# Kernel optimization log

Measured on AMD Instinct MI355X. Metric: run time of the kernel, lower is better.

The kernel has to match this reference:

```python
import jax, jax.numpy as jnp
import numpy as np

B, E, H, NC = 16384, 1024, 8, 32
FF = 4 * E

def _ln(x, g, b, eps=1e-5):
    m = jnp.mean(x, -1, keepdims=True)
    v = jnp.mean((x - m) ** 2, -1, keepdims=True)
    return (x - m) * jax.lax.rsqrt(v + eps) * g + b

def _mha1(q_in, kv_in, Wq, Wk, Wv, bq, bk, bv, Wo, bo):
    # seq_len == 1 for both query and key/value; x: [B, E]
    Bn = q_in.shape[0]
    dh = E // H
    q = (q_in @ Wq.T + bq).reshape(Bn, H, dh)
    k = (kv_in @ Wk.T + bk).reshape(Bn, H, dh)
    v = (kv_in @ Wv.T + bv).reshape(Bn, H, dh)
    s = jnp.sum(q * k, -1, keepdims=True) / np.float32(np.sqrt(dh))  # [B,H,1]
    w = jax.nn.softmax(s, axis=-1)  # single key -> weights == 1 exactly
    o = (w * v).reshape(Bn, E)
    return o @ Wo.T + bo

def _ffn(x, W1, b1, W2, b2):
    h = jax.nn.gelu(x @ W1.T + b1, approximate=False)  # torch GELU = exact erf
    return h @ W2.T + b2

def setup_inputs():
    key = jax.random.key(0)
    ks = iter(jax.random.split(key, 64))
    def w(shape, s=0.02):
        return jax.random.normal(next(ks), shape, jnp.float32) * s
    z = lambda n: jnp.zeros((n,), jnp.float32)
    o = lambda n: jnp.ones((n,), jnp.float32)
    d = {
        'lc_cls': jax.random.normal(next(ks), (B, E), jnp.float32),
        'tab_embedding': jax.random.normal(next(ks), (B, E), jnp.float32),
        'ln_lc_g': o(E), 'ln_lc_b': z(E),
        'ln_tab_g': o(E), 'ln_tab_b': z(E),
    }
    for p in ('alc', 'atab'):
        d[p + '_Wq'] = w((E, E)); d[p + '_Wk'] = w((E, E)); d[p + '_Wv'] = w((E, E))
        d[p + '_bq'] = z(E); d[p + '_bk'] = z(E); d[p + '_bv'] = z(E)
        d[p + '_Wo'] = w((E, E)); d[p + '_bo'] = z(E)
    for p in ('flc', 'ftab'):
        d[p + '_W1'] = w((FF, E)); d[p + '_b1'] = z(FF)
        d[p + '_W2'] = w((E, FF)); d[p + '_b2'] = z(E)
    d['on_g'] = o(2 * E); d['on_b'] = z(2 * E)
    d['c_W1'] = w((E, 2 * E)); d['c_b1'] = z(E)
    d['c_ln_g'] = o(E); d['c_ln_b'] = z(E)
    d['c_W2'] = w((NC, E)); d['c_b2'] = z(NC)
    return d

def reference(lc_cls, tab_embedding, ln_lc_g, ln_lc_b, ln_tab_g, ln_tab_b,
              alc_Wq, alc_Wk, alc_Wv, alc_bq, alc_bk, alc_bv, alc_Wo, alc_bo,
              atab_Wq, atab_Wk, atab_Wv, atab_bq, atab_bk, atab_bv, atab_Wo, atab_bo,
              flc_W1, flc_b1, flc_W2, flc_b2, ftab_W1, ftab_b1, ftab_W2, ftab_b2,
              on_g, on_b, c_W1, c_b1, c_ln_g, c_ln_b, c_W2, c_b2):
    # dropout is identity at inference
    lc_n = _ln(lc_cls, ln_lc_g, ln_lc_b)
    tab_n = _ln(tab_embedding, ln_tab_g, ln_tab_b)
    lc_cross = lc_cls + _mha1(lc_n, tab_n, alc_Wq, alc_Wk, alc_Wv, alc_bq, alc_bk, alc_bv, alc_Wo, alc_bo)
    tab_cross = tab_embedding + _mha1(tab_n, lc_n, atab_Wq, atab_Wk, atab_Wv, atab_bq, atab_bk, atab_bv, atab_Wo, atab_bo)
    lc_out = lc_cross + _ffn(lc_cross, flc_W1, flc_b1, flc_W2, flc_b2)
    tab_out = tab_cross + _ffn(tab_cross, ftab_W1, ftab_b1, ftab_W2, ftab_b2)
    fused = _ln(jnp.concatenate([lc_out, tab_out], axis=1), on_g, on_b)
    h = jax.nn.gelu(_ln(fused @ c_W1.T + c_b1, c_ln_g, c_ln_b), approximate=False)
    return h @ c_W2.T + c_b2
```

## Files before the change

kernel.cpp:

```cpp
#include <hip/hip_runtime.h>
#include <hip/hip_bf16.h>
#include <math.h>

typedef __bf16 bf16_t;
typedef __bf16 bf16x8 __attribute__((ext_vector_type(8)));
typedef __bf16 bf16x4 __attribute__((ext_vector_type(4)));
typedef float  f32x4  __attribute__((ext_vector_type(4)));

#define NB   16384
#define EDIM 1024
#define FFD  4096
#define NCD  32

__device__ __forceinline__ float gelu_exact(float x) {
    return 0.5f * x * (1.0f + erff(x * 0.70710678118654752f));
}

__device__ __forceinline__ void gload16(const bf16_t* g, bf16_t* l) {
    __builtin_amdgcn_global_load_lds(
        (__attribute__((address_space(1))) void*)(g),
        (__attribute__((address_space(3))) void*)(l),
        16, 0, 0);
}

enum { EPI_PLAIN = 0, EPI_RESF32 = 1, EPI_GELU = 2, EPI_RESBF16 = 3 };

struct GemmArgs {
    const bf16_t* A0; const bf16_t* A1;
    const bf16_t* B0; const bf16_t* B1;
    const float*  bias0; const float* bias1;
    const void*   res0; const void*  res1;
    bf16_t*       out0; bf16_t*      out1;
};

template<int EPI>
__global__ __launch_bounds__(512, 2)
void gemm256(GemmArgs g, int ldo, int co0, int co1, int M, int N, int K)
{
    __shared__ bf16_t lds[65536];

    const int side = blockIdx.z;
    const bf16_t* __restrict__ A    = side ? g.A1   : g.A0;
    const bf16_t* __restrict__ Bw   = side ? g.B1   : g.B0;
    const float*  __restrict__ bias = side ? g.bias1: g.bias0;
    const void*   __restrict__ resid= side ? g.res1 : g.res0;
    bf16_t*       __restrict__ out  = side ? g.out1 : g.out0;
    const int coloff = side ? co1 : co0;

    const int nx = gridDim.x;
    const int nwg = nx * gridDim.y;
    int lin = blockIdx.y * nx + blockIdx.x;
    {
        const int q = nwg >> 3, r = nwg & 7;
        const int xc = lin & 7, ix = lin >> 3;
        lin = (xc < r ? xc * (q + 1) : r * (q + 1) + (xc - r) * q) + ix;
    }
    const long bm = (long)(lin / nx) * 256;
    const long bn = (long)(lin % nx) * 256;

    const int tid = threadIdx.x, lane = tid & 63, wave = tid >> 6;
    const int wm = wave >> 2, wn = wave & 3;
    const int fr = lane & 15;
    const int sphys = ((lane >> 4) ^ (fr & 3) ^ ((fr >> 2) & 3)) * 8;
    const int abase = (wm * 128 + fr) * 32 + sphys;
    const int bbase = (wn * 64  + fr) * 32 + sphys;

    const int rowl = tid >> 2;
    const int scol = ((tid & 3) ^ (rowl & 3) ^ ((rowl >> 2) & 3)) * 8;
    const bf16_t* gA0 = A  + (bm + rowl)       * (long)K + scol;
    const bf16_t* gA1 = A  + (bm + 128 + rowl) * (long)K + scol;
    const bf16_t* gB0 = Bw + (bn + rowl)       * (long)K + scol;
    const bf16_t* gB1 = Bw + (bn + 128 + rowl) * (long)K + scol;
    bf16_t* const l0 = lds + wave * 512;

    const int nt = K >> 5;
    auto stage = [&](int ts, int bufi) {
        const long ko = (long)ts << 5;
        bf16_t* d = l0 + bufi * 16384;
        gload16(gA0 + ko, d);
        gload16(gA1 + ko, d + 4096);
        gload16(gB0 + ko, d + 8192);
        gload16(gB1 + ko, d + 12288);
    };
    stage(0, 0);
    stage(nt > 1 ? 1 : nt - 1, 1);
    stage(nt > 2 ? 2 : nt - 1, 2);

    f32x4 acc[8][4] = {};

    for (int t = 0; t < nt; ++t) {
        asm volatile("s_waitcnt vmcnt(8)" ::: "memory");
        __builtin_amdgcn_s_barrier();
        asm volatile("" ::: "memory");

        int ts = t + 3; if (ts >= nt) ts = nt - 1;
        stage(ts, (t + 3) & 3);

        const bf16_t* bA = lds + (t & 3) * 16384;
        const bf16_t* bB = bA + 8192;

        bf16x8 bfr[4], afr[4];
        #pragma unroll
        for (int ni = 0; ni < 4; ++ni) bfr[ni] = *(const bf16x8*)(bB + bbase + ni * 512);
        #pragma unroll
        for (int mi = 0; mi < 4; ++mi) afr[mi] = *(const bf16x8*)(bA + abase + mi * 512);
        __builtin_amdgcn_s_setprio(1);
        #pragma unroll
        for (int mi = 0; mi < 4; ++mi)
            #pragma unroll
            for (int ni = 0; ni < 4; ++ni)
                acc[mi][ni] = __builtin_amdgcn_mfma_f32_16x16x32_bf16(
                                  afr[mi], bfr[ni], acc[mi][ni], 0, 0, 0);
        __builtin_amdgcn_s_setprio(0);
        #pragma unroll
        for (int mi = 0; mi < 4; ++mi) afr[mi] = *(const bf16x8*)(bA + abase + 2048 + mi * 512);
        __builtin_amdgcn_s_setprio(1);
        #pragma unroll
        for (int mi = 0; mi < 4; ++mi)
            #pragma unroll
            for (int ni = 0; ni < 4; ++ni)
                acc[4 + mi][ni] = __builtin_amdgcn_mfma_f32_16x16x32_bf16(
                                  afr[mi], bfr[ni], acc[4 + mi][ni], 0, 0, 0);
        __builtin_amdgcn_s_setprio(0);
    }

    const int rq = (lane >> 4) * 4;
    #pragma unroll
    for (int mi = 0; mi < 8; ++mi) {
        #pragma unroll
        for (int ni = 0; ni < 4; ++ni) {
            const long n = bn + wn * 64 + ni * 16 + fr;
            const float bval = bias ? bias[n] : 0.0f;
            #pragma unroll
            for (int r = 0; r < 4; ++r) {
                const long m = bm + wm * 128 + mi * 16 + rq + r;
                float v = acc[mi][ni][r] + bval;
                if (EPI == EPI_RESF32)  v += ((const float*)resid)[m * (long)N + n];
                if (EPI == EPI_RESBF16) v += (float)((const bf16_t*)resid)[m * (long)N + n];
                if (EPI == EPI_GELU)    v = gelu_exact(v);
                out[m * (long)ldo + coloff + n] = (bf16_t)v;
            }
        }
    }
}

template<int EPI>
__global__ __launch_bounds__(256)
void gemm128(GemmArgs g, int ldo, int co0, int co1, int M, int N, int K)
{
    __shared__ bf16_t sA[128 * 32];
    __shared__ bf16_t sB[128 * 32];

    const int side = blockIdx.z;
    const bf16_t* __restrict__ A    = side ? g.A1   : g.A0;
    const bf16_t* __restrict__ Bw   = side ? g.B1   : g.B0;
    const float*  __restrict__ bias = side ? g.bias1: g.bias0;
    const void*   __restrict__ resid= side ? g.res1 : g.res0;
    bf16_t*       __restrict__ out  = side ? g.out1 : g.out0;
    const int coloff = side ? co1 : co0;

    const int nx = gridDim.x;
    const int nwg = nx * gridDim.y;
    int lin = blockIdx.y * nx + blockIdx.x;
    {
        const int q = nwg >> 3, r = nwg & 7;
        const int xc = lin & 7, ix = lin >> 3;
        lin = (xc < r ? xc * (q + 1) : r * (q + 1) + (xc - r) * q) + ix;
    }
    const long bm = (long)(lin / nx) * 128;
    const long bn = (long)(lin % nx) * 128;

    const int tid  = threadIdx.x;
    const int lane = tid & 63;
    const int wave = tid >> 6;
    const int wr = (wave >> 1) * 64;
    const int wc = (wave & 1) * 64;

    const int srow = lane >> 2;
    const int scol = (lane & 3) * 8;
    const int r0   = wave * 32;

    const bf16_t* gA = A  + (bm + r0 + srow) * (long)K + scol;
    const bf16_t* gB = Bw + (bn + r0 + srow) * (long)K + scol;
    bf16_t* lA = sA + r0 * 32;
    bf16_t* lB = sB + r0 * 32;

    const int fr = lane & 15;
    const int fk = (lane >> 4) * 8;
    const bf16_t* rA = sA + (wr + fr) * 32 + fk;
    const bf16_t* rB = sB + (wc + fr) * 32 + fk;

    f32x4 acc[4][4] = {};

    for (int kt = 0; kt < K; kt += 32) {
        gload16(gA + kt,                lA);
        gload16(gA + kt + 16 * (long)K, lA + 16 * 32);
        gload16(gB + kt,                lB);
        gload16(gB + kt + 16 * (long)K, lB + 16 * 32);
        __syncthreads();

        bf16x8 av[4], bv[4];
        #pragma unroll
        for (int i = 0; i < 4; ++i) {
            av[i] = *(const bf16x8*)(rA + i * 16 * 32);
            bv[i] = *(const bf16x8*)(rB + i * 16 * 32);
        }
        #pragma unroll
        for (int mi = 0; mi < 4; ++mi)
            #pragma unroll
            for (int ni = 0; ni < 4; ++ni)
                acc[mi][ni] = __builtin_amdgcn_mfma_f32_16x16x32_bf16(
                                  av[mi], bv[ni], acc[mi][ni], 0, 0, 0);
        __syncthreads();
    }

    const int rq = (lane >> 4) * 4;
    #pragma unroll
    for (int mi = 0; mi < 4; ++mi) {
        #pragma unroll
        for (int ni = 0; ni < 4; ++ni) {
            const long n = bn + wc + ni * 16 + fr;
            const float bval = bias ? bias[n] : 0.0f;
            #pragma unroll
            for (int r = 0; r < 4; ++r) {
                const long m = bm + wr + mi * 16 + rq + r;
                float v = acc[mi][ni][r] + bval;
                if (EPI == EPI_RESF32)  v += ((const float*)resid)[m * (long)N + n];
                if (EPI == EPI_RESBF16) v += (float)((const bf16_t*)resid)[m * (long)N + n];
                if (EPI == EPI_GELU)    v = gelu_exact(v);
                out[m * (long)ldo + coloff + n] = (bf16_t)v;
            }
        }
    }
}

__global__ __launch_bounds__(256)
void final_mfma(const bf16_t* __restrict__ U, const bf16_t* __restrict__ W2,
                const float* __restrict__ b2, float* __restrict__ out)
{
    __shared__ bf16_t sA[128 * 32];
    __shared__ bf16_t sB[32 * 32];
    const int tid = threadIdx.x, lane = tid & 63, wave = tid >> 6;
    const long bm = (long)blockIdx.x * 128;
    const int srow = lane >> 2, scol = (lane & 3) * 8;

    const bf16_t* gA = U + (bm + wave * 32 + srow) * (long)EDIM + scol;
    bf16_t* lA = sA + wave * 32 * 32;
    const bf16_t* gB = W2 + ((long)wave * 16 + srow) * EDIM + scol;
    bf16_t* lB = sB + wave * 16 * 32;

    const int fr = lane & 15, fk = (lane >> 4) * 8;
    const bf16_t* rA = sA + (wave * 32 + fr) * 32 + fk;
    const bf16_t* rB = sB + fr * 32 + fk;

    f32x4 acc[2][2] = {};
    for (int kt = 0; kt < EDIM; kt += 32) {
        gload16(gA + kt,             lA);
        gload16(gA + kt + 16 * EDIM, lA + 16 * 32);
        if (wave < 2) gload16(gB + kt, lB);
        __syncthreads();
        bf16x8 av[2], bv[2];
        av[0] = *(const bf16x8*)(rA);
        av[1] = *(const bf16x8*)(rA + 16 * 32);
        bv[0] = *(const bf16x8*)(rB);
        bv[1] = *(const bf16x8*)(rB + 16 * 32);
        #pragma unroll
        for (int mi = 0; mi < 2; ++mi)
            #pragma unroll
            for (int ni = 0; ni < 2; ++ni)
                acc[mi][ni] = __builtin_amdgcn_mfma_f32_16x16x32_bf16(
                                  av[mi], bv[ni], acc[mi][ni], 0, 0, 0);
        __syncthreads();
    }
    const int rq = (lane >> 4) * 4;
    #pragma unroll
    for (int mi = 0; mi < 2; ++mi)
        #pragma unroll
        for (int ni = 0; ni < 2; ++ni) {
            const int n = ni * 16 + fr;
            const float bval = b2[n];
            #pragma unroll
            for (int r = 0; r < 4; ++r) {
                const long m = bm + wave * 32 + mi * 16 + rq + r;
                out[m * NCD + n] = acc[mi][ni][r] + bval;
            }
        }
}

__global__ __launch_bounds__(256)
void ln_f32(const float* __restrict__ X, const float* __restrict__ g,
            const float* __restrict__ b, bf16_t* __restrict__ out)
{
    const long row = blockIdx.x;
    const int t = threadIdx.x;
    f32x4 x = ((const f32x4*)(X + row * EDIM))[t];
    float s = x[0] + x[1] + x[2] + x[3];
    float q = x[0]*x[0] + x[1]*x[1] + x[2]*x[2] + x[3]*x[3];
    #pragma unroll
    for (int off = 32; off; off >>= 1) { s += __shfl_xor(s, off); q += __shfl_xor(q, off); }
    __shared__ float red[8];
    if ((t & 63) == 0) { red[(t >> 6) * 2] = s; red[(t >> 6) * 2 + 1] = q; }
    __syncthreads();
    s = red[0] + red[2] + red[4] + red[6];
    q = red[1] + red[3] + red[5] + red[7];
    const float mean = s * (1.0f / EDIM);
    const float rs = rsqrtf(q * (1.0f / EDIM) - mean * mean + 1e-5f);
    f32x4 gg = ((const f32x4*)g)[t];
    f32x4 bb = ((const f32x4*)b)[t];
    bf16x4 o;
    #pragma unroll
    for (int j = 0; j < 4; ++j) o[j] = (bf16_t)((x[j] - mean) * rs * gg[j] + bb[j]);
    ((bf16x4*)(out + row * EDIM))[t] = o;
}

__global__ __launch_bounds__(256)
void ln_cat(const bf16_t* __restrict__ X, const float* __restrict__ g,
            const float* __restrict__ b, bf16_t* __restrict__ out)
{
    const long row = blockIdx.x;
    const int t = threadIdx.x;
    bf16x8 xv = ((const bf16x8*)(X + row * 2048))[t];
    float xf[8];
    float s = 0.f, q = 0.f;
    #pragma unroll
    for (int j = 0; j < 8; ++j) { xf[j] = (float)xv[j]; s += xf[j]; q += xf[j] * xf[j]; }
    #pragma unroll
    for (int off = 32; off; off >>= 1) { s += __shfl_xor(s, off); q += __shfl_xor(q, off); }
    __shared__ float red[8];
    if ((t & 63) == 0) { red[(t >> 6) * 2] = s; red[(t >> 6) * 2 + 1] = q; }
    __syncthreads();
    s = red[0] + red[2] + red[4] + red[6];
    q = red[1] + red[3] + red[5] + red[7];
    const float mean = s * (1.0f / 2048);
    const float rs = rsqrtf(q * (1.0f / 2048) - mean * mean + 1e-5f);
    f32x4 g0 = ((const f32x4*)g)[2 * t], g1 = ((const f32x4*)g)[2 * t + 1];
    f32x4 b0 = ((const f32x4*)b)[2 * t], b1 = ((const f32x4*)b)[2 * t + 1];
    bf16x8 o;
    #pragma unroll
    for (int j = 0; j < 4; ++j) o[j]     = (bf16_t)((xf[j]     - mean) * rs * g0[j] + b0[j]);
    #pragma unroll
    for (int j = 0; j < 4; ++j) o[4 + j] = (bf16_t)((xf[4 + j] - mean) * rs * g1[j] + b1[j]);
    ((bf16x8*)(out + row * 2048))[t] = o;
}

__global__ __launch_bounds__(256)
void ln_gelu(const bf16_t* __restrict__ X, const float* __restrict__ g,
             const float* __restrict__ b, bf16_t* __restrict__ out)
{
    const long row = blockIdx.x;
    const int t = threadIdx.x;
    bf16x4 xv = ((const bf16x4*)(X + row * EDIM))[t];
    float xf[4];
    float s = 0.f, q = 0.f;
    #pragma unroll
    for (int j = 0; j < 4; ++j) { xf[j] = (float)xv[j]; s += xf[j]; q += xf[j] * xf[j]; }
    #pragma unroll
    for (int off = 32; off; off >>= 1) { s += __shfl_xor(s, off); q += __shfl_xor(q, off); }
    __shared__ float red[8];
    if ((t & 63) == 0) { red[(t >> 6) * 2] = s; red[(t >> 6) * 2 + 1] = q; }
    __syncthreads();
    s = red[0] + red[2] + red[4] + red[6];
    q = red[1] + red[3] + red[5] + red[7];
    const float mean = s * (1.0f / EDIM);
    const float rs = rsqrtf(q * (1.0f / EDIM) - mean * mean + 1e-5f);
    f32x4 gg = ((const f32x4*)g)[t];
    f32x4 bb = ((const f32x4*)b)[t];
    bf16x4 o;
    #pragma unroll
    for (int j = 0; j < 4; ++j)
        o[j] = (bf16_t)gelu_exact((xf[j] - mean) * rs * gg[j] + bb[j]);
    ((bf16x4*)(out + row * EDIM))[t] = o;
}

__global__ void f2b(const float* __restrict__ in, bf16_t* __restrict__ out, long n4)
{
    long i = (long)blockIdx.x * blockDim.x + threadIdx.x;
    const long stride = (long)gridDim.x * blockDim.x;
    for (; i < n4; i += stride) {
        f32x4 v = ((const f32x4*)in)[i];
        bf16x4 o;
        #pragma unroll
        for (int j = 0; j < 4; ++j) o[j] = (bf16_t)v[j];
        ((bf16x4*)out)[i] = o;
    }
}

__global__ void tconv(const float* __restrict__ in, bf16_t* __restrict__ out)
{
    const long x = (long)blockIdx.x * 256 + threadIdx.x;
    const int k = (int)(x & (EDIM - 1));
    const int j = (int)(x >> 10);
    out[(long)j * EDIM + k] = (bf16_t)in[(long)k * EDIM + j];
}

__global__ __launch_bounds__(256)
void bcomb_k(const float* __restrict__ Wo, const float* __restrict__ bv,
             const float* __restrict__ bo, float* __restrict__ bc)
{
    const int i = blockIdx.x;
    const int t = threadIdx.x;
    f32x4 w = ((const f32x4*)(Wo + (long)i * EDIM))[t];
    f32x4 v = ((const f32x4*)bv)[t];
    float s = w[0]*v[0] + w[1]*v[1] + w[2]*v[2] + w[3]*v[3];
    #pragma unroll
    for (int off = 32; off; off >>= 1) s += __shfl_xor(s, off);
    __shared__ float red[4];
    if ((t & 63) == 0) red[t >> 6] = s;
    __syncthreads();
    if (t == 0) bc[i] = red[0] + red[1] + red[2] + red[3] + bo[i];
}

extern "C" void kernel_launch(void* const* d_in, const int* in_sizes, int n_in,
                              void* d_out, int out_size, void* d_ws, size_t ws_size,
                              hipStream_t stream)
{
    const float* lc_cls   = (const float*)d_in[0];
    const float* tab_emb  = (const float*)d_in[1];
    const float* ln_lc_g  = (const float*)d_in[2];
    const float* ln_lc_b  = (const float*)d_in[3];
    const float* ln_tab_g = (const float*)d_in[4];
    const float* ln_tab_b = (const float*)d_in[5];
    const float* alc_Wv   = (const float*)d_in[8];
    const float* alc_bv   = (const float*)d_in[11];
    const float* alc_Wo   = (const float*)d_in[12];
    const float* alc_bo   = (const float*)d_in[13];
    const float* atab_Wv  = (const float*)d_in[16];
    const float* atab_bv  = (const float*)d_in[19];
    const float* atab_Wo  = (const float*)d_in[20];
    const float* atab_bo  = (const float*)d_in[21];
    const float* flc_W1   = (const float*)d_in[22];
    const float* flc_b1   = (const float*)d_in[23];
    const float* flc_W2   = (const float*)d_in[24];
    const float* flc_b2   = (const float*)d_in[25];
    const float* ftab_W1  = (const float*)d_in[26];
    const float* ftab_b1  = (const float*)d_in[27];
    const float* ftab_W2  = (const float*)d_in[28];
    const float* ftab_b2  = (const float*)d_in[29];
    const float* on_g     = (const float*)d_in[30];
    const float* on_b     = (const float*)d_in[31];
    const float* c_W1     = (const float*)d_in[32];
    const float* c_b1     = (const float*)d_in[33];
    const float* c_ln_g   = (const float*)d_in[34];
    const float* c_ln_b   = (const float*)d_in[35];
    const float* c_W2     = (const float*)d_in[36];
    const float* c_b2     = (const float*)d_in[37];

    char* ws = (char*)d_ws;
    size_t woff = 0;
    auto walloc = [&](size_t bytes) {
        void* p = ws + woff;
        woff += (bytes + 255) & ~(size_t)255;
        return p;
    };
    bf16_t* Wc_lc  = (bf16_t*)walloc((size_t)EDIM * EDIM * 2);
    bf16_t* Wc_tab = (bf16_t*)walloc((size_t)EDIM * EDIM * 2);
    bf16_t* W1lc_b = (bf16_t*)walloc((size_t)FFD * EDIM * 2);
    bf16_t* W2lc_b = (bf16_t*)walloc((size_t)EDIM * FFD * 2);
    bf16_t* W1tab_b= (bf16_t*)walloc((size_t)FFD * EDIM * 2);
    bf16_t* W2tab_b= (bf16_t*)walloc((size_t)EDIM * FFD * 2);
    bf16_t* cW1_b  = (bf16_t*)walloc((size_t)EDIM * 2 * EDIM * 2);
    bf16_t* cW2_b  = (bf16_t*)walloc((size_t)NCD * EDIM * 2);
    float*  bc_lc  = (float*)walloc(EDIM * 4);
    float*  bc_tab = (float*)walloc(EDIM * 4);

    char* arena = ws + woff;
    const size_t arena_sz = (ws_size > woff) ? (ws_size - woff) : 0;

    int SB = NB;
    while (SB > 256 && (size_t)SB * 24576 > arena_sz) SB >>= 1;
    if ((size_t)SB * 24576 > arena_sz) return;

    const size_t S2 = (size_t)SB * 2048;
    bf16_t* lc_n  = (bf16_t*)(arena);
    bf16_t* tab_n = (bf16_t*)(arena + S2);
    bf16_t* cat   = (bf16_t*)(arena);
    bf16_t* lc_x  = (bf16_t*)(arena + 2 * S2);
    bf16_t* tab_x = (bf16_t*)(arena + 3 * S2);
    bf16_t* hbuf0 = (bf16_t*)(arena + 4 * S2);
    bf16_t* hbuf1 = (bf16_t*)(arena + 8 * S2);
    bf16_t* tbuf  = lc_x;
    bf16_t* ubuf  = tab_x;

    bf16_t* Wo_lc_b  = (bf16_t*)(arena);
    bf16_t* Wo_tab_b = (bf16_t*)(arena + (size_t)2 * 1024 * 1024);
    bf16_t* WvT_lc   = (bf16_t*)(arena + (size_t)4 * 1024 * 1024);
    bf16_t* WvT_tab  = (bf16_t*)(arena + (size_t)6 * 1024 * 1024);

    f2b<<<512, 256, 0, stream>>>(alc_Wo,  Wo_lc_b,  (long)EDIM * EDIM / 4);
    f2b<<<512, 256, 0, stream>>>(atab_Wo, Wo_tab_b, (long)EDIM * EDIM / 4);
    tconv<<<EDIM * EDIM / 256, 256, 0, stream>>>(alc_Wv,  WvT_lc);
    tconv<<<EDIM * EDIM / 256, 256, 0, stream>>>(atab_Wv, WvT_tab);
    f2b<<<2048, 256, 0, stream>>>(flc_W1,  W1lc_b,  (long)FFD * EDIM / 4);
    f2b<<<2048, 256, 0, stream>>>(flc_W2,  W2lc_b,  (long)EDIM * FFD / 4);
    f2b<<<2048, 256, 0, stream>>>(ftab_W1, W1tab_b, (long)FFD * EDIM / 4);
    f2b<<<2048, 256, 0, stream>>>(ftab_W2, W2tab_b, (long)EDIM * FFD / 4);
    f2b<<<1024, 256, 0, stream>>>(c_W1,    cW1_b,   (long)EDIM * 2 * EDIM / 4);
    f2b<<<32,   256, 0, stream>>>(c_W2,    cW2_b,   (long)NCD * EDIM / 4);
    bcomb_k<<<EDIM, 256, 0, stream>>>(alc_Wo,  alc_bv,  alc_bo,  bc_lc);
    bcomb_k<<<EDIM, 256, 0, stream>>>(atab_Wo, atab_bv, atab_bo, bc_tab);
    {
        GemmArgs ga = { Wo_lc_b, Wo_tab_b, WvT_lc, WvT_tab,
                        nullptr, nullptr, nullptr, nullptr, Wc_lc, Wc_tab };
        gemm128<EPI_PLAIN><<<dim3(EDIM/128, EDIM/128, 2), 256, 0, stream>>>(
            ga, EDIM, 0, 0, EDIM, EDIM, EDIM);
    }

    for (long c0 = 0; c0 < NB; c0 += SB) {
        const float* lcI  = lc_cls  + c0 * EDIM;
        const float* tabI = tab_emb + c0 * EDIM;

        ln_f32<<<SB, 256, 0, stream>>>(lcI,  ln_lc_g,  ln_lc_b,  lc_n);
        ln_f32<<<SB, 256, 0, stream>>>(tabI, ln_tab_g, ln_tab_b, tab_n);

        {
            GemmArgs ga = { tab_n, lc_n, Wc_lc, Wc_tab, bc_lc, bc_tab,
                            lcI, tabI, lc_x, tab_x };
            gemm256<EPI_RESF32><<<dim3(EDIM/256, SB/256, 2), 512, 0, stream>>>(
                ga, EDIM, 0, 0, SB, EDIM, EDIM);
        }
        {
            GemmArgs ga = { lc_x, tab_x, W1lc_b, W1tab_b, flc_b1, ftab_b1,
                            nullptr, nullptr, hbuf0, hbuf1 };
            gemm256<EPI_GELU><<<dim3(FFD/256, SB/256, 2), 512, 0, stream>>>(
                ga, FFD, 0, 0, SB, FFD, EDIM);
        }
        {
            GemmArgs ga = { hbuf0, hbuf1, W2lc_b, W2tab_b, flc_b2, ftab_b2,
                            lc_x, tab_x, cat, cat };
            gemm256<EPI_RESBF16><<<dim3(EDIM/256, SB/256, 2), 512, 0, stream>>>(
                ga, 2 * EDIM, 0, EDIM, SB, EDIM, FFD);
        }

        ln_cat<<<SB, 256, 0, stream>>>(cat, on_g, on_b, cat);

        {
            GemmArgs ga = { cat, cat, cW1_b, cW1_b, c_b1, c_b1,
                            nullptr, nullptr, tbuf, tbuf };
            gemm128<EPI_PLAIN><<<dim3(EDIM/128, SB/128, 1), 256, 0, stream>>>(
                ga, EDIM, 0, 0, SB, EDIM, 2 * EDIM);
        }
        ln_gelu<<<SB, 256, 0, stream>>>(tbuf, c_ln_g, c_ln_b, ubuf);
        final_mfma<<<SB / 128, 256, 0, stream>>>(ubuf, cW2_b, c_b2,
                                                 (float*)d_out + c0 * NCD);
    }
}
```

Before: 1.144 ms.

## Rewrite 256x256 GEMM mainloop as 8-phase ping-pong with K=64 tiles

Replaces the 4-buffer K=32 pipelined GEMM with a K=64 tile scheme. The loop is split into four compute phases separated by barriers, and global-to-LDS loads for future half-tiles are interleaved between the MFMA phases using a new XOR swizzle. The aim is to overlap memory traffic with MFMA work more finely and halve the loop trip count. The classifier's first GEMM also moves from the 128-tile kernel to the new 256-tile kernel, and the 128 kernel drops its block remapping. The extra barriers add synchronisation overhead, and the intricate buffer-slot and vmcnt accounting carries correctness risk.

Measured after the change: 1.170 ms. +2.2%, slower.

```diff
diff --git a/kernel.cpp b/kernel.cpp
--- a/kernel.cpp
+++ b/kernel.cpp
@@ -22,6 +22,10 @@
         (__attribute__((address_space(3))) void*)(l),
         16, 0, 0);
 }
+
+#define PH_BAR() do { asm volatile("" ::: "memory"); \
+                      __builtin_amdgcn_s_barrier();  \
+                      asm volatile("" ::: "memory"); } while (0)
 
 enum { EPI_PLAIN = 0, EPI_RESF32 = 1, EPI_GELU = 2, EPI_RESBF16 = 3 };
 
@@ -35,9 +39,10 @@
 
 template<int EPI>
 __global__ __launch_bounds__(512, 2)
-void gemm256(GemmArgs g, int ldo, int co0, int co1, int M, int N, int K)
-{
-    __shared__ bf16_t lds[65536];
+void gemm8p(GemmArgs g, int ldo, int co0, int co1, int M, int N, int K)
+{
+    __shared__ __align__(128) bf16_t lds[65536];
+    char* const ldsb = (char*)lds;
 
     const int side = blockIdx.z;
     const bf16_t* __restrict__ A    = side ? g.A1   : g.A0;
@@ -60,68 +65,124 @@
 
     const int tid = threadIdx.x, lane = tid & 63, wave = tid >> 6;
     const int wm = wave >> 2, wn = wave & 3;
-    const int fr = lane & 15;
-    const int sphys = ((lane >> 4) ^ (fr & 3) ^ ((fr >> 2) & 3)) * 8;
-    const int abase = (wm * 128 + fr) * 32 + sphys;
-    const int bbase = (wn * 64  + fr) * 32 + sphys;
-
-    const int rowl = tid >> 2;
-    const int scol = ((tid & 3) ^ (rowl & 3) ^ ((rowl >> 2) & 3)) * 8;
-    const bf16_t* gA0 = A  + (bm + rowl)       * (long)K + scol;
-    const bf16_t* gA1 = A  + (bm + 128 + rowl) * (long)K + scol;
-    const bf16_t* gB0 = Bw + (bn + rowl)       * (long)K + scol;
-    const bf16_t* gB1 = Bw + (bn + 128 + rowl) * (long)K + scol;
-    bf16_t* const l0 = lds + wave * 512;
-
-    const int nt = K >> 5;
-    auto stage = [&](int ts, int bufi) {
-        const long ko = (long)ts << 5;
-        bf16_t* d = l0 + bufi * 16384;
-        gload16(gA0 + ko, d);
-        gload16(gA1 + ko, d + 4096);
-        gload16(gB0 + ko, d + 8192);
-        gload16(gB1 + ko, d + 12288);
+    const int fr = lane & 15, ks = lane >> 4;
+    const int xl = (fr >> 2) & 3;
+    const int colb0 = ((((ks >> 1) + 0) ^ xl) << 5) | ((ks & 1) << 4);
+    const int colb1 = ((((ks >> 1) + 2) ^ xl) << 5) | ((ks & 1) << 4);
+
+    const int xs = ((wave << 1) + (lane >> 5)) & 3;
+    const int sc8 = ((lane & 7) ^ (xs << 1)) * 8;
+    auto STAGE = [&](const bf16_t* __restrict__ Op, long ldk, long row0, long kcol,
+                     int slotbyte) {
+        #pragma unroll
+        for (int i = 0; i < 2; ++i) {
+            const int r = i * 64 + wave * 8 + (lane >> 3);
+            gload16(Op + (row0 + r) * ldk + kcol + sc8,
+                    (bf16_t*)(ldsb + slotbyte + (i * 512 + wave * 64) * 16));
+        }
     };
-    stage(0, 0);
-    stage(nt > 1 ? 1 : nt - 1, 1);
-    stage(nt > 2 ? 2 : nt - 1, 2);
 
     f32x4 acc[8][4] = {};
+    const int nt = K >> 6;
+
+    STAGE(A,  K, bm,        0, 0 * 16384);
+    STAGE(A,  K, bm + 128,  0, 1 * 16384);
+    STAGE(Bw, K, bn,        0, 65536 + 0 * 16384);
+    STAGE(Bw, K, bn + 128,  0, 65536 + 1 * 16384);
+    if (nt > 1) {
+        STAGE(Bw, K, bn,       64, 65536 + 2 * 16384);
+        STAGE(Bw, K, bn + 128, 64, 65536 + 3 * 16384);
+        STAGE(A,  K, bm,       64, 2 * 16384);
+        asm volatile("s_waitcnt vmcnt(6)" ::: "memory");
+    } else {
+        asm volatile("s_waitcnt vmcnt(0)" ::: "memory");
+    }
+    PH_BAR();
 
     for (int t = 0; t < nt; ++t) {
-        asm volatile("s_waitcnt vmcnt(8)" ::: "memory");
-        __builtin_amdgcn_s_barrier();
-        asm volatile("" ::: "memory");
-
-        int ts = t + 3; if (ts >= nt) ts = nt - 1;
-        stage(ts, (t + 3) & 3);
-
-        const bf16_t* bA = lds + (t & 3) * 16384;
-        const bf16_t* bB = bA + 8192;
-
-        bf16x8 bfr[4], afr[4];
-        #pragma unroll
-        for (int ni = 0; ni < 4; ++ni) bfr[ni] = *(const bf16x8*)(bB + bbase + ni * 512);
-        #pragma unroll
-        for (int mi = 0; mi < 4; ++mi) afr[mi] = *(const bf16x8*)(bA + abase + mi * 512);
+        const char* aB = ldsb + (((2 * t + wm) & 3) << 14);
+        const char* bB = ldsb + 65536 + (((2 * t + (wn >> 1)) & 3) << 14);
+        bf16x8 a0[4][2], a1[4][2], b0[2][2], b1[2][2];
+
+        #pragma unroll
+        for (int mi = 0; mi < 4; ++mi) {
+            a0[mi][0] = *(const bf16x8*)(aB + (mi * 16 + fr) * 128 + colb0);
+            a0[mi][1] = *(const bf16x8*)(aB + (mi * 16 + fr) * 128 + colb1);
+        }
+        #pragma unroll
+        for (int ni = 0; ni < 2; ++ni) {
+            b0[ni][0] = *(const bf16x8*)(bB + ((wn & 1) * 64 + ni * 16 + fr) * 128 + colb0);
+            b0[ni][1] = *(const bf16x8*)(bB + ((wn & 1) * 64 + ni * 16 + fr) * 128 + colb1);
+        }
+        if (t + 1 < nt) STAGE(A, K, bm + 128, (long)(t + 1) * 64, ((2 * t + 3) & 3) << 14);
+        PH_BAR();
         __builtin_amdgcn_s_setprio(1);
         #pragma unroll
         for (int mi = 0; mi < 4; ++mi)
             #pragma unroll
-            for (int ni = 0; ni < 4; ++ni)
-                acc[mi][ni] = __builtin_amdgcn_mfma_f32_16x16x32_bf16(
-                                  afr[mi], bfr[ni], acc[mi][ni], 0, 0, 0);
+            for (int ni = 0; ni < 2; ++ni)
+                #pragma unroll
+                for (int kk = 0; kk < 2; ++kk)
+                    acc[mi][ni] = __builtin_amdgcn_mfma_f32_16x16x32_bf16(
+                        a0[mi][kk], b0[ni][kk], acc[mi][ni], 0, 0, 0);
         __builtin_amdgcn_s_setprio(0);
-        #pragma unroll
-        for (int mi = 0; mi < 4; ++mi) afr[mi] = *(const bf16x8*)(bA + abase + 2048 + mi * 512);
+        PH_BAR();
+
+        #pragma unroll
+        for (int ni = 0; ni < 2; ++ni) {
+            b1[ni][0] = *(const bf16x8*)(bB + ((wn & 1) * 64 + 32 + ni * 16 + fr) * 128 + colb0);
+            b1[ni][1] = *(const bf16x8*)(bB + ((wn & 1) * 64 + 32 + ni * 16 + fr) * 128 + colb1);
+        }
+        PH_BAR();
         __builtin_amdgcn_s_setprio(1);
         #pragma unroll
         for (int mi = 0; mi < 4; ++mi)
             #pragma unroll
-            for (int ni = 0; ni < 4; ++ni)
-                acc[4 + mi][ni] = __builtin_amdgcn_mfma_f32_16x16x32_bf16(
-                                  afr[mi], bfr[ni], acc[4 + mi][ni], 0, 0, 0);
+            for (int ni = 0; ni < 2; ++ni)
+                #pragma unroll
+                for (int kk = 0; kk < 2; ++kk)
+                    acc[mi][2 + ni] = __builtin_amdgcn_mfma_f32_16x16x32_bf16(
+                        a0[mi][kk], b1[ni][kk], acc[mi][2 + ni], 0, 0, 0);
         __builtin_amdgcn_s_setprio(0);
+        PH_BAR();
+
+        #pragma unroll
+        for (int mi = 0; mi < 4; ++mi) {
+            a1[mi][0] = *(const bf16x8*)(aB + (64 + mi * 16 + fr) * 128 + colb0);
+            a1[mi][1] = *(const bf16x8*)(aB + (64 + mi * 16 + fr) * 128 + colb1);
+        }
+        if (t + 2 < nt) {
+            STAGE(Bw, K, bn,       (long)(t + 2) * 64, 65536 + (((2 * t) & 3) << 14));
+            STAGE(Bw, K, bn + 128, (long)(t + 2) * 64, 65536 + (((2 * t + 1) & 3) << 14));
+        }
+        PH_BAR();
+        __builtin_amdgcn_s_setprio(1);
+        #pragma unroll
+        for (int mi = 0; mi < 4; ++mi)
+            #pragma unroll
+            for (int ni = 0; ni < 2; ++ni)
+                #pragma unroll
+                for (int kk = 0; kk < 2; ++kk)
+                    acc[4 + mi][ni] = __builtin_amdgcn_mfma_f32_16x16x32_bf16(
+                        a1[mi][kk], b0[ni][kk], acc[4 + mi][ni], 0, 0, 0);
+        __builtin_amdgcn_s_setprio(0);
+        PH_BAR();
+
+        if (t + 2 < nt) STAGE(A, K, bm, (long)(t + 2) * 64, ((2 * t) & 3) << 14);
+        PH_BAR();
+        __builtin_amdgcn_s_setprio(1);
+        #pragma unroll
+        for (int mi = 0; mi < 4; ++mi)
+            #pragma unroll
+            for (int ni = 0; ni < 2; ++ni)
+                #pragma unroll
+                for (int kk = 0; kk < 2; ++kk)
+                    acc[4 + mi][2 + ni] = __builtin_amdgcn_mfma_f32_16x16x32_bf16(
+                        a1[mi][kk], b1[ni][kk], acc[4 + mi][2 + ni], 0, 0, 0);
+        __builtin_amdgcn_s_setprio(0);
+        if (t + 2 < nt) { asm volatile("s_waitcnt vmcnt(6)" ::: "memory"); }
+        else            { asm volatile("s_waitcnt vmcnt(0)" ::: "memory"); }
+        PH_BAR();
     }
 
     const int rq = (lane >> 4) * 4;
@@ -159,16 +220,8 @@
     bf16_t*       __restrict__ out  = side ? g.out1 : g.out0;
     const int coloff = side ? co1 : co0;
 
-    const int nx = gridDim.x;
-    const int nwg = nx * gridDim.y;
-    int lin = blockIdx.y * nx + blockIdx.x;
-    {
-        const int q = nwg >> 3, r = nwg & 7;
-        const int xc = lin & 7, ix = lin >> 3;
-        lin = (xc < r ? xc * (q + 1) : r * (q + 1) + (xc - r) * q) + ix;
-    }
-    const long bm = (long)(lin / nx) * 128;
-    const long bn = (long)(lin % nx) * 128;
+    const long bm = (long)blockIdx.y * 128;
+    const long bn = (long)blockIdx.x * 128;
 
     const int tid  = threadIdx.x;
     const int lane = tid & 63;
@@ -515,19 +568,19 @@
         {
             GemmArgs ga = { tab_n, lc_n, Wc_lc, Wc_tab, bc_lc, bc_tab,
                             lcI, tabI, lc_x, tab_x };
-            gemm256<EPI_RESF32><<<dim3(EDIM/256, SB/256, 2), 512, 0, stream>>>(
+            gemm8p<EPI_RESF32><<<dim3(EDIM/256, SB/256, 2), 512, 0, stream>>>(
                 ga, EDIM, 0, 0, SB, EDIM, EDIM);
         }
         {
             GemmArgs ga = { lc_x, tab_x, W1lc_b, W1tab_b, flc_b1, ftab_b1,
                             nullptr, nullptr, hbuf0, hbuf1 };
-            gemm256<EPI_GELU><<<dim3(FFD/256, SB/256, 2), 512, 0, stream>>>(
+            gemm8p<EPI_GELU><<<dim3(FFD/256, SB/256, 2), 512, 0, stream>>>(
                 ga, FFD, 0, 0, SB, FFD, EDIM);
         }
         {
             GemmArgs ga = { hbuf0, hbuf1, W2lc_b, W2tab_b, flc_b2, ftab_b2,
                             lc_x, tab_x, cat, cat };
-            gemm256<EPI_RESBF16><<<dim3(EDIM/256, SB/256, 2), 512, 0, stream>>>(
+            gemm8p<EPI_RESBF16><<<dim3(EDIM/256, SB/256, 2), 512, 0, stream>>>(
                 ga, 2 * EDIM, 0, EDIM, SB, EDIM, FFD);
         }
 
@@ -536,7 +589,7 @@
         {
             GemmArgs ga = { cat, cat, cW1_b, cW1_b, c_b1, c_b1,
                             nullptr, nullptr, tbuf, tbuf };
-            gemm128<EPI_PLAIN><<<dim3(EDIM/128, SB/128, 1), 256, 0, stream>>>(
+            gemm8p<EPI_PLAIN><<<dim3(EDIM/256, SB/256, 1), 512, 0, stream>>>(
                 ga, EDIM, 0, 0, SB, EDIM, 2 * EDIM);
         }
         ln_gelu<<<SB, 256, 0, stream>>>(tbuf, c_ln_g, c_ln_b, ubuf);
```
